# Kernel optimization log

Hardware: AMD Instinct MI355X
Metric: run time of the kernel (lower is better)

The kernel has to match this reference:

```python
import jax, jax.numpy as jnp
import numpy as np

NEG = -1e30  # log-space 'zero'


def setup_inputs() -> dict:
    N, T, IDIM, V, S = 16, 1024, 512, 4096, 128
    key = jax.random.key(0)
    k0, k1, k2, k3, k4 = jax.random.split(key, 5)
    hs = jax.random.normal(k0, (N, T, IDIM), dtype=jnp.float32)
    hlens = jax.random.randint(k1, (N,), T // 2, T + 1).astype(jnp.int32)
    ys = jax.random.randint(k2, (N, S), 1, V).astype(jnp.int32)  # labels exclude blank=0
    ylens = jax.random.randint(k3, (N,), S // 2, S + 1).astype(jnp.int32)
    W = jax.random.normal(k4, (V, IDIM), dtype=jnp.float32) * 0.02
    b = jnp.zeros((V,), dtype=jnp.float32)
    return {"hs": hs, "hlens": hlens, "ys": ys, "ylens": ylens, "W": W, "b": b}


def _ctc_loss(logp, hlens, ys, ylens):
    # logp: (N, T, V) log-softmax outputs; blank index = 0
    N, T, V = logp.shape
    S = ys.shape[1]
    L = 2 * S + 1
    # extended label sequence: blank, y1, blank, y2, ..., blank
    ext = jnp.zeros((N, L), dtype=ys.dtype).at[:, 1::2].set(ys)  # (N, L)
    s_idx = jnp.arange(L)
    ext_prev2 = jnp.pad(ext, ((0, 0), (2, 0)))[:, :L]
    allow_skip = (ext != 0) & (ext != ext_prev2) & (s_idx[None, :] >= 2)  # (N, L)
    Ln = 2 * ylens + 1  # valid extended length per sample

    lpT = jnp.swapaxes(logp, 0, 1)  # (T, N, V)

    # t = 0 init
    alpha0 = jnp.full((N, L), NEG, dtype=logp.dtype)
    alpha0 = alpha0.at[:, 0].set(lpT[0, :, 0])
    alpha0 = alpha0.at[:, 1].set(jnp.take_along_axis(lpT[0], ys[:, :1], axis=1)[:, 0])

    def step(alpha, xs):
        lp_t, t = xs  # lp_t: (N, V)
        lp_ext = jnp.take_along_axis(lp_t, ext, axis=1)  # (N, L)
        a1 = alpha
        a2 = jnp.pad(alpha, ((0, 0), (1, 0)), constant_values=NEG)[:, :L]
        a3 = jnp.pad(alpha, ((0, 0), (2, 0)), constant_values=NEG)[:, :L]
        a3 = jnp.where(allow_skip, a3, NEG)
        new = jnp.logaddexp(jnp.logaddexp(a1, a2), a3) + lp_ext
        new = jnp.where(s_idx[None, :] < Ln[:, None], new, NEG)
        alpha = jnp.where((t < hlens)[:, None], new, alpha)
        return alpha, None

    ts = jnp.arange(1, T, dtype=hlens.dtype)
    alpha, _ = jax.lax.scan(step, alpha0, (lpT[1:], ts))

    end1 = jnp.take_along_axis(alpha, (Ln - 1)[:, None], axis=1)[:, 0]
    end2 = jnp.take_along_axis(alpha, (Ln - 2)[:, None], axis=1)[:, 0]
    ll = jnp.logaddexp(end1, end2)  # (N,)
    per = jnp.where(ll > -1e29, -ll, 0.0)  # zero_infinity=True
    return jnp.sum(per) / N  # reduction='sum' then divided by len(hlens)


def reference(hs, hlens, ys, ylens, W, b):
    logits = jnp.einsum('nti,vi->ntv', hs, W) + b  # (N, T, V)
    logp = jax.nn.log_softmax(logits, axis=-1)
    return _ctc_loss(logp, hlens, ys, ylens)
```

## Files before the change

kernel.cpp:

```cpp
#include <hip/hip_runtime.h>
#include <cstdint>
#include <cstddef>

using short8_t = __attribute__((ext_vector_type(8))) short;
using f32x4    = __attribute__((ext_vector_type(4))) float;
typedef unsigned short bfu16;

constexpr int   Nn   = 16;
constexpr int   Tt   = 1024;
constexpr int   IDIM = 512;
constexpr int   Vv   = 4096;
constexpr int   Ss   = 128;
constexpr int   Ll   = 2 * Ss + 1;
constexpr int   LS   = 132;
constexpr float NEGV = -1e30f;
constexpr float L2E  = 1.4426950408889634f;
constexpr float LN2  = 0.6931471805599453f;

__device__ __forceinline__ float fexp2(float x) { return __builtin_amdgcn_exp2f(x); }
__device__ __forceinline__ float flog2(float x) { return __builtin_amdgcn_logf(x); }

__device__ __forceinline__ bfu16 f2bf(float f) {
  unsigned int x = __float_as_uint(f);
  x = x + 0x7fffu + ((x >> 16) & 1u);
  return (bfu16)(x >> 16);
}

__device__ __forceinline__ void async16(const void* g, void* l) {
  __builtin_amdgcn_global_load_lds(
      (__attribute__((address_space(1))) void*)(g),
      (__attribute__((address_space(3))) void*)(l), 16, 0, 0);
}

__global__ void convert_zero(const float4* __restrict__ hs4,
                             const float4* __restrict__ W4,
                             ushort4* __restrict__ hsb4,
                             ushort4* __restrict__ Wb4,
                             float* __restrict__ out) {
  if (blockIdx.x == 0 && threadIdx.x == 0) out[0] = 0.f;
  const int HS4 = (Nn * Tt * IDIM) / 4;
  const int TOT = HS4 + (Vv * IDIM) / 4;
  for (int i = blockIdx.x * 256 + threadIdx.x; i < TOT; i += gridDim.x * 256) {
    float4 f;
    if (i < HS4) f = hs4[i]; else f = W4[i - HS4];
    ushort4 o;
    o.x = f2bf(f.x); o.y = f2bf(f.y); o.z = f2bf(f.z); o.w = f2bf(f.w);
    if (i < HS4) hsb4[i] = o; else Wb4[i - HS4] = o;
  }
}

__global__ void build_labels(const int* __restrict__ ys,
                             int* __restrict__ labmap,
                             int* __restrict__ extidx,
                             int* __restrict__ skipflag) {
  const int n = blockIdx.x, tid = threadIdx.x;
  int* lm = labmap + n * Vv;
  for (int v = tid; v < Vv; v += 256) lm[v] = 0x7fffffff;
  __syncthreads();
  if (tid == 0) lm[0] = 0;
  if (tid < Ss) atomicMin(&lm[ys[n * Ss + tid]], tid + 1);
  __syncthreads();
  for (int s = tid; s < Ll; s += 256) {
    int v = (s & 1) ? ys[n * Ss + ((s - 1) >> 1)] : 0;
    extidx[n * Ll + s] = lm[v];
    int allow = 0;
    if ((s & 1) && s >= 3) allow = (v != ys[n * Ss + ((s - 3) >> 1)]) ? 1 : 0;
    skipflag[n * Ll + s] = allow;
  }
  __syncthreads();
  for (int v = tid; v < Vv; v += 256)
    if (lm[v] == 0x7fffffff) lm[v] = -1;
}

__global__ __launch_bounds__(512, 2) void gemm_lse(
    const bfu16* __restrict__ A,
    const bfu16* __restrict__ B,
    const float* __restrict__ bias,
    const int*   __restrict__ labmap,
    float* __restrict__ plab,
    float* __restrict__ psum) {
  __shared__ alignas(128) char ldsraw[131072];
  const int tid  = threadIdx.x;
  const int lane = tid & 63, wid = tid >> 6;
  const int wr = wid >> 2, wc = wid & 3;

  const int flat = blockIdx.x;
  const int wg   = (flat & 7) * 128 + (flat >> 3);
  const int bR = wg >> 4, bC = wg & 15;
  const int rowbase = bR * 256, colbase = bC * 256;

  f32x4 acc[8][4];
#pragma unroll
  for (int m = 0; m < 8; m++)
#pragma unroll
    for (int n = 0; n < 4; n++) {
      f32x4 z = {0.f, 0.f, 0.f, 0.f};
      acc[m][n] = z;
    }

  const int  sw  = wid & 3;
  const bool isB = wid >= 4;
  const char* gsrc0 = (const char*)(isB ? (const void*)B : (const void*)A)
      + (size_t)((isB ? colbase : rowbase) + sw * 64 + (lane >> 3)) * (IDIM * 2)
      + (((lane & 7) ^ ((lane >> 3) & 7)) * 16);
  char* ldst0 = ldsraw + (isB ? 32768 : 0) + sw * 8192;

  const int fr = lane & 15;
  const int g  = lane >> 4;
  const int fx = fr & 7;

  const int nsamp = bR >> 2;
  const int* lm = labmap + nsamp * Vv;
  float bc[4];
  int   slot[4];
#pragma unroll
  for (int n = 0; n < 4; n++) {
    int c = colbase + wc * 64 + n * 16 + fr;
    bc[n]   = bias[c];
    slot[n] = lm[c];
  }

  auto stage = [&](int b, int t) {
#pragma unroll
    for (int i = 0; i < 8; ++i)
      async16(gsrc0 + (size_t)t * 128 + i * 8192, ldst0 + b * 65536 + i * 1024);
  };

  stage(0, 0);
  asm volatile("s_waitcnt vmcnt(0)" ::: "memory");
  __builtin_amdgcn_s_barrier();

  int buf = 0;
  for (int t = 0; t < 8; ++t) {
    const char* Ab = ldsraw + buf * 65536;
    const char* Bb = Ab + 32768;
    if (t < 7) stage(buf ^ 1, t + 1);

    short8_t a0[4], a1[4], a2[4], a3[4], b0[4], b1[4];
#pragma unroll
    for (int m = 0; m < 4; m++)
      a0[m] = *(const short8_t*)(Ab + (wr * 128 + m * 16 + fr) * 128 + ((0 + g) ^ fx) * 16);
#pragma unroll
    for (int n = 0; n < 4; n++)
      b0[n] = *(const short8_t*)(Bb + (wc * 64 + n * 16 + fr) * 128 + ((0 + g) ^ fx) * 16);
#pragma unroll
    for (int m = 0; m < 4; m++)
      a1[m] = *(const short8_t*)(Ab + (wr * 128 + (m + 4) * 16 + fr) * 128 + ((0 + g) ^ fx) * 16);

    __builtin_amdgcn_s_setprio(1);
#pragma unroll
    for (int m = 0; m < 4; m++)
#pragma unroll
      for (int n = 0; n < 4; n++)
        acc[m][n] = __builtin_amdgcn_mfma_f32_16x16x32_bf16(a0[m], b0[n], acc[m][n], 0, 0, 0);
    __builtin_amdgcn_s_setprio(0);

#pragma unroll
    for (int m = 0; m < 4; m++)
      a2[m] = *(const short8_t*)(Ab + (wr * 128 + m * 16 + fr) * 128 + ((4 + g) ^ fx) * 16);
#pragma unroll
    for (int n = 0; n < 4; n++)
      b1[n] = *(const short8_t*)(Bb + (wc * 64 + n * 16 + fr) * 128 + ((4 + g) ^ fx) * 16);

    __builtin_amdgcn_s_setprio(1);
#pragma unroll
    for (int m = 0; m < 4; m++)
#pragma unroll
      for (int n = 0; n < 4; n++)
        acc[m + 4][n] = __builtin_amdgcn_mfma_f32_16x16x32_bf16(a1[m], b0[n], acc[m + 4][n], 0, 0, 0);
    __builtin_amdgcn_s_setprio(0);

#pragma unroll
    for (int m = 0; m < 4; m++)
      a3[m] = *(const short8_t*)(Ab + (wr * 128 + (m + 4) * 16 + fr) * 128 + ((4 + g) ^ fx) * 16);

    __builtin_amdgcn_s_setprio(1);
#pragma unroll
    for (int m = 0; m < 4; m++)
#pragma unroll
      for (int n = 0; n < 4; n++)
        acc[m][n] = __builtin_amdgcn_mfma_f32_16x16x32_bf16(a2[m], b1[n], acc[m][n], 0, 0, 0);
    __builtin_amdgcn_s_setprio(0);

    __builtin_amdgcn_s_setprio(1);
#pragma unroll
    for (int m = 0; m < 4; m++)
#pragma unroll
      for (int n = 0; n < 4; n++)
        acc[m + 4][n] = __builtin_amdgcn_mfma_f32_16x16x32_bf16(a3[m], b1[n], acc[m + 4][n], 0, 0, 0);
    __builtin_amdgcn_s_setprio(0);

    asm volatile("s_waitcnt vmcnt(0)" ::: "memory");
    __builtin_amdgcn_s_barrier();
    buf ^= 1;
  }

  const int g4 = g * 4;
#pragma unroll
  for (int m = 0; m < 8; m++) {
#pragma unroll
    for (int r = 0; r < 4; r++) {
      int row = rowbase + wr * 128 + m * 16 + g4 + r;
      float e0 = fexp2((acc[m][0][r] + bc[0]) * L2E);
      float e1 = fexp2((acc[m][1][r] + bc[1]) * L2E);
      float e2 = fexp2((acc[m][2][r] + bc[2]) * L2E);
      float e3 = fexp2((acc[m][3][r] + bc[3]) * L2E);
      if (slot[0] >= 0) plab[(size_t)row * LS + slot[0]] = e0;
      if (slot[1] >= 0) plab[(size_t)row * LS + slot[1]] = e1;
      if (slot[2] >= 0) plab[(size_t)row * LS + slot[2]] = e2;
      if (slot[3] >= 0) plab[(size_t)row * LS + slot[3]] = e3;
      float s = (e0 + e1) + (e2 + e3);
      s += __shfl_xor(s, 1);
      s += __shfl_xor(s, 2);
      s += __shfl_xor(s, 4);
      s += __shfl_xor(s, 8);
      if (fr == 0) {
        int pc = bC * 4 + wc;
        psum[(size_t)pc * 16384 + row] = s;
      }
    }
  }
}

__global__ void lse_reduce(const float* __restrict__ psum,
                           float* __restrict__ lse) {
  int row = blockIdx.x * 256 + threadIdx.x;
  float s = 0.f;
#pragma unroll 8
  for (int j = 0; j < 64; j++)
    s += psum[(size_t)j * 16384 + row];
  lse[row] = flog2(s) * LN2;
}

constexpr int DPD = 8;

__global__ __launch_bounds__(64) void ctc_dp(
    const float* __restrict__ plab, const float* __restrict__ lse,
    const int* __restrict__ extidx, const int* __restrict__ skipflag,
    const int* __restrict__ hlens, const int* __restrict__ ylens,
    float* __restrict__ out) {
  const int n    = blockIdx.x;
  const int lane = threadIdx.x;
  const int hlen = hlens[n];
  const int Ln   = 2 * ylens[n] + 1;
  const int sbase = lane * 4;

  const int   e1  = extidx[n * Ll + sbase + 1];
  const int   e3  = extidx[n * Ll + sbase + 3];
  const float sk1 = skipflag[n * Ll + sbase + 1] ? 1.f : 0.f;
  const float sk3 = skipflag[n * Ll + sbase + 3] ? 1.f : 0.f;
  const float m0  = (sbase + 0 < Ln) ? 1.f : 0.f;
  const float m1  = (sbase + 1 < Ln) ? 1.f : 0.f;
  const float m2  = (sbase + 2 < Ln) ? 1.f : 0.f;
  const float m3  = (sbase + 3 < Ln) ? 1.f : 0.f;
  const float m4  = (lane == 63 && Ln == 257) ? 1.f : 0.f;

  const float* pl  = plab + (size_t)n * Tt * LS;
  const float* lsp = lse + n * Tt;

  float slse = 0.f;
  for (int t = lane; t < hlen; t += 64) slse += lsp[t];
#pragma unroll
  for (int off = 32; off; off >>= 1) slse += __shfl_xor(slse, off);

  float a0 = 0.f, a1 = 0.f, a2 = 0.f, a3 = 0.f, a4 = 0.f;
  if (lane == 0) { a0 = pl[0]; a1 = pl[e1]; }

  int sc = 0;

  auto step = [&](float pb, float p1, float p3) {
    float pm1 = __shfl_up(a3, 1);
    float pm2 = __shfl_up(a2, 1);
    pm1 = (lane == 0) ? 0.f : pm1;
    pm2 = (lane == 0) ? 0.f : pm2;
    float n4 = (a4 + a3) * pb * m4;
    float n3 = (a3 + a2 + sk3 * a1)  * p3 * m3;
    float n2 = (a2 + a1)             * pb * m2;
    float n1 = (a1 + a0 + sk1 * pm2) * p1 * m1;
    float n0 = (a0 + pm1)            * pb * m0;
    a0 = n0; a1 = n1; a2 = n2; a3 = n3; a4 = n4;
  };

  auto rescale = [&]() {
    float mx = fmaxf(fmaxf(a0, a1), fmaxf(a2, a3));
    mx = fmaxf(mx, a4);
#pragma unroll
    for (int off = 32; off; off >>= 1) mx = fmaxf(mx, __shfl_xor(mx, off));
    int ee = (int)((__float_as_uint(mx) >> 23) & 0xff) - 127;
    ee = (mx > 0.f) ? ee : 0;
    float s = __uint_as_float((unsigned)(127 - ee) << 23);
    sc += ee;
    a0 *= s; a1 *= s; a2 *= s; a3 *= s; a4 *= s;
  };

  float rb[DPD], r1[DPD], r3[DPD];
#pragma unroll
  for (int d = 0; d < DPD; d++) {
    int tt = 1 + d;
    rb[d] = pl[(size_t)tt * LS];
    r1[d] = pl[(size_t)tt * LS + e1];
    r3[d] = pl[(size_t)tt * LS + e3];
  }

  const int nfull = (hlen - 1) / DPD;
  for (int b = 0; b < nfull; b++) {
    const int t0 = 1 + b * DPD;
#pragma unroll
    for (int d = 0; d < DPD; d++) {
      float pb = rb[d], p1 = r1[d], p3 = r3[d];
      int tn = t0 + d + DPD;
      if (tn > Tt - 1) tn = Tt - 1;
      rb[d] = pl[(size_t)tn * LS];
      r1[d] = pl[(size_t)tn * LS + e1];
      r3[d] = pl[(size_t)tn * LS + e3];
      step(pb, p1, p3);
    }
    if ((b & 1) || b == nfull - 1) rescale();
  }
  for (int t = 1 + nfull * DPD; t < hlen; t++) {
    step(pl[(size_t)t * LS], pl[(size_t)t * LS + e1], pl[(size_t)t * LS + e3]);
  }

  __shared__ float alf[264];
  alf[sbase + 0] = a0; alf[sbase + 1] = a1;
  alf[sbase + 2] = a2; alf[sbase + 3] = a3;
  if (lane == 63) alf[256] = a4;
  __syncthreads();
  if (lane == 0) {
    float sum = alf[Ln - 1] + alf[Ln - 2];
    float per = 0.f;
    if (sum > 0.f) {
      float llv = (flog2(sum) + (float)sc) * LN2 - slse;
      if (llv > -1e29f) per = -llv;
    }
    atomicAdd(out, per * (1.0f / 16.0f));
  }
}

extern "C" void kernel_launch(void* const* d_in, const int* in_sizes, int n_in,
                              void* d_out, int out_size, void* d_ws, size_t ws_size,
                              hipStream_t stream) {
  const float* hs    = (const float*)d_in[0];
  const int*   hlens = (const int*)d_in[1];
  const int*   ys    = (const int*)d_in[2];
  const int*   ylens = (const int*)d_in[3];
  const float* W     = (const float*)d_in[4];
  const float* bias  = (const float*)d_in[5];
  float*       out   = (float*)d_out;
  char*        ws    = (char*)d_ws;

  const size_t off_hsb    = 0;
  const size_t off_Wb     = off_hsb    + (size_t)Nn*Tt*IDIM*2;
  const size_t off_plab   = off_Wb     + (size_t)Vv*IDIM*2;
  const size_t off_psum   = off_plab   + (size_t)Nn*Tt*LS*4;
  const size_t off_lse    = off_psum   + (size_t)64*16384*4;
  const size_t off_labmap = off_lse    + (size_t)16384*4;
  const size_t off_extidx = off_labmap + (size_t)Nn*Vv*4;
  const size_t off_skip   = off_extidx + (size_t)((Nn*Ll*4 + 255) & ~255);

  bfu16* hsb    = (bfu16*)(ws + off_hsb);
  bfu16* Wb     = (bfu16*)(ws + off_Wb);
  float* plab   = (float*)(ws + off_plab);
  float* psum   = (float*)(ws + off_psum);
  float* lse    = (float*)(ws + off_lse);
  int*   labmap = (int*)(ws + off_labmap);
  int*   extidx = (int*)(ws + off_extidx);
  int*   skipf  = (int*)(ws + off_skip);

  convert_zero<<<2048, 256, 0, stream>>>(
      (const float4*)hs, (const float4*)W, (ushort4*)hsb, (ushort4*)Wb, out);
  build_labels<<<16, 256, 0, stream>>>(ys, labmap, extidx, skipf);
  gemm_lse<<<1024, 512, 0, stream>>>(hsb, Wb, bias, labmap, plab, psum);
  lse_reduce<<<64, 256, 0, stream>>>(psum, lse);
  ctc_dp<<<16, 64, 0, stream>>>(plab, lse, extidx, skipf, hlens, ylens, out);
}
```

Before: 211.1 us.

## Fuse two CTC time steps per cross-lane exchange and defer length masking

The CTC alpha recursion now advances two time steps per iteration. Each lane fetches its neighbours' previous-step values (plus one neighbour emission) with cross-lane shuffles and computes the halo term locally, so the shuffle round-trip on the serial critical path happens once per two steps instead of once per step. Per-step validity-mask multiplies move into the periodic rescale, on the reasoning that states past the valid length never feed back into valid states. The lse sum loop is also fully unrolled with predication. The cost is more arithmetic per iteration and four shuffles per pair instead of two per step; the logic is subtle because masking is now delayed.

```diff
diff --git a/kernel.cpp b/kernel.cpp
--- a/kernel.cpp
+++ b/kernel.cpp
@@ -232,7 +232,7 @@
   lse[row] = flog2(s) * LN2;
 }
 
-constexpr int DPD = 8;
+constexpr int DP2 = 4;
 
 __global__ __launch_bounds__(64) void ctc_dp(
     const float* __restrict__ plab, const float* __restrict__ lse,
@@ -249,6 +249,8 @@
   const int   e3  = extidx[n * Ll + sbase + 3];
   const float sk1 = skipflag[n * Ll + sbase + 1] ? 1.f : 0.f;
   const float sk3 = skipflag[n * Ll + sbase + 3] ? 1.f : 0.f;
+  const float skh = (lane > 0 && skipflag[n * Ll + sbase - 1]) ? 1.f : 0.f;
+  const bool  l0  = (lane == 0);
   const float m0  = (sbase + 0 < Ln) ? 1.f : 0.f;
   const float m1  = (sbase + 1 < Ln) ? 1.f : 0.f;
   const float m2  = (sbase + 2 < Ln) ? 1.f : 0.f;
@@ -259,29 +261,55 @@
   const float* lsp = lse + n * Tt;
 
   float slse = 0.f;
-  for (int t = lane; t < hlen; t += 64) slse += lsp[t];
+#pragma unroll
+  for (int j = 0; j < 16; j++) {
+    int t = lane + 64 * j;
+    float v = lsp[t];
+    slse += (t < hlen) ? v : 0.f;
+  }
 #pragma unroll
   for (int off = 32; off; off >>= 1) slse += __shfl_xor(slse, off);
 
   float a0 = 0.f, a1 = 0.f, a2 = 0.f, a3 = 0.f, a4 = 0.f;
-  if (lane == 0) { a0 = pl[0]; a1 = pl[e1]; }
+  if (l0) { a0 = pl[0]; a1 = pl[e1]; }
 
   int sc = 0;
 
-  auto step = [&](float pb, float p1, float p3) {
+  auto pair2 = [&](float pbA, float p1A, float p3A,
+                   float pbB, float p1B, float p3B) {
+    float pa3 = __shfl_up(a3, 1);
+    float pa2 = __shfl_up(a2, 1);
+    float pa1 = __shfl_up(a1, 1);
+    float prA = __shfl_up(p3A, 1);
+    pa3 = l0 ? 0.f : pa3;
+    pa2 = l0 ? 0.f : pa2;
+    pa1 = l0 ? 0.f : pa1;
+    float h1 = (pa3 + pa2 + skh * pa1) * prA;
+    float s4 = (a4 + a3) * pbA;
+    float s3 = (a3 + a2 + sk3 * a1) * p3A;
+    float s2 = (a2 + a1) * pbA;
+    float s1 = (a1 + a0 + sk1 * pa3) * p1A;
+    float s0 = (a0 + pa3) * pbA;
+    a4 = (s4 + s3) * pbB;
+    a3 = (s3 + s2 + sk3 * s1) * p3B;
+    a2 = (s2 + s1) * pbB;
+    a1 = (s1 + s0 + sk1 * h1) * p1B;
+    a0 = (s0 + h1) * pbB;
+  };
+
+  auto step1 = [&](float pb, float p1, float p3) {
     float pm1 = __shfl_up(a3, 1);
-    float pm2 = __shfl_up(a2, 1);
-    pm1 = (lane == 0) ? 0.f : pm1;
-    pm2 = (lane == 0) ? 0.f : pm2;
-    float n4 = (a4 + a3) * pb * m4;
-    float n3 = (a3 + a2 + sk3 * a1)  * p3 * m3;
-    float n2 = (a2 + a1)             * pb * m2;
-    float n1 = (a1 + a0 + sk1 * pm2) * p1 * m1;
-    float n0 = (a0 + pm1)            * pb * m0;
+    pm1 = l0 ? 0.f : pm1;
+    float n4 = (a4 + a3) * pb;
+    float n3 = (a3 + a2 + sk3 * a1) * p3;
+    float n2 = (a2 + a1) * pb;
+    float n1 = (a1 + a0 + sk1 * pm1) * p1;
+    float n0 = (a0 + pm1) * pb;
     a0 = n0; a1 = n1; a2 = n2; a3 = n3; a4 = n4;
   };
 
   auto rescale = [&]() {
+    a0 *= m0; a1 *= m1; a2 *= m2; a3 *= m3; a4 *= m4;
     float mx = fmaxf(fmaxf(a0, a1), fmaxf(a2, a3));
     mx = fmaxf(mx, a4);
 #pragma unroll
@@ -293,40 +321,58 @@
     a0 *= s; a1 *= s; a2 *= s; a3 *= s; a4 *= s;
   };
 
-  float rb[DPD], r1[DPD], r3[DPD];
-#pragma unroll
-  for (int d = 0; d < DPD; d++) {
-    int tt = 1 + d;
-    rb[d] = pl[(size_t)tt * LS];
-    r1[d] = pl[(size_t)tt * LS + e1];
-    r3[d] = pl[(size_t)tt * LS + e3];
-  }
-
-  const int nfull = (hlen - 1) / DPD;
-  for (int b = 0; b < nfull; b++) {
-    const int t0 = 1 + b * DPD;
-#pragma unroll
-    for (int d = 0; d < DPD; d++) {
-      float pb = rb[d], p1 = r1[d], p3 = r3[d];
-      int tn = t0 + d + DPD;
-      if (tn > Tt - 1) tn = Tt - 1;
-      rb[d] = pl[(size_t)tn * LS];
-      r1[d] = pl[(size_t)tn * LS + e1];
-      r3[d] = pl[(size_t)tn * LS + e3];
-      step(pb, p1, p3);
+  const int nsteps = hlen - 1;
+  const int npairs = nsteps >> 1;
+
+  float rbA[DP2], r1A[DP2], r3A[DP2], rbB[DP2], r1B[DP2], r3B[DP2];
+#pragma unroll
+  for (int d = 0; d < DP2; d++) {
+    int tA = 1 + 2 * d, tB = tA + 1;
+    rbA[d] = pl[(size_t)tA * LS];
+    r1A[d] = pl[(size_t)tA * LS + e1];
+    r3A[d] = pl[(size_t)tA * LS + e3];
+    rbB[d] = pl[(size_t)tB * LS];
+    r1B[d] = pl[(size_t)tB * LS + e1];
+    r3B[d] = pl[(size_t)tB * LS + e3];
+  }
+
+  const int nblk = npairs / DP2;
+  for (int b = 0; b < nblk; b++) {
+#pragma unroll
+    for (int d = 0; d < DP2; d++) {
+      float pbA = rbA[d], p1A = r1A[d], p3A = r3A[d];
+      float pbB = rbB[d], p1B = r1B[d], p3B = r3B[d];
+      int jn = b * DP2 + d + DP2;
+      int tA = 1 + 2 * jn, tB = tA + 1;
+      if (tA > Tt - 1) tA = Tt - 1;
+      if (tB > Tt - 1) tB = Tt - 1;
+      rbA[d] = pl[(size_t)tA * LS];
+      r1A[d] = pl[(size_t)tA * LS + e1];
+      r3A[d] = pl[(size_t)tA * LS + e3];
+      rbB[d] = pl[(size_t)tB * LS];
+      r1B[d] = pl[(size_t)tB * LS + e1];
+      r3B[d] = pl[(size_t)tB * LS + e3];
+      pair2(pbA, p1A, p3A, pbB, p1B, p3B);
     }
-    if ((b & 1) || b == nfull - 1) rescale();
-  }
-  for (int t = 1 + nfull * DPD; t < hlen; t++) {
-    step(pl[(size_t)t * LS], pl[(size_t)t * LS + e1], pl[(size_t)t * LS + e3]);
-  }
+    if ((b & 1) || b == nblk - 1) rescale();
+  }
+  for (int j = nblk * DP2; j < npairs; j++) {
+    int tA = 1 + 2 * j, tB = tA + 1;
+    pair2(pl[(size_t)tA * LS], pl[(size_t)tA * LS + e1], pl[(size_t)tA * LS + e3],
+          pl[(size_t)tB * LS], pl[(size_t)tB * LS + e1], pl[(size_t)tB * LS + e3]);
+  }
+  if (nsteps & 1) {
+    int t = nsteps;
+    step1(pl[(size_t)t * LS], pl[(size_t)t * LS + e1], pl[(size_t)t * LS + e3]);
+  }
+  rescale();
 
   __shared__ float alf[264];
   alf[sbase + 0] = a0; alf[sbase + 1] = a1;
   alf[sbase + 2] = a2; alf[sbase + 3] = a3;
   if (lane == 63) alf[256] = a4;
   __syncthreads();
-  if (lane == 0) {
+  if (l0) {
     float sum = alf[Ln - 1] + alf[Ln - 2];
     float per = 0.f;
     if (sum > 0.f) {
```

New measurement: 205.2 us. 2.8% less time.
